# Kernel tuning notes

Measured on AMD Instinct MI355X. Metric: run time of the kernel, lower is better.

The kernel has to match this reference:

```python
import jax, jax.numpy as jnp
import numpy as np

N = 50000      # num nodes
E = 800000     # num edges
IN_C = 256
OUT_C = 128


def setup_inputs() -> dict:
    key = jax.random.key(0)
    k1, k2, k3, k4 = jax.random.split(key, 4)
    x = jax.random.normal(k1, (N, IN_C), dtype=jnp.float32)
    edge_index = jax.random.randint(k2, (2, E), 0, N, dtype=jnp.int64)
    # Linear params (Kaiming-uniform-ish scale like torch Linear reset)
    bound = 1.0 / np.sqrt(IN_C)
    W = jax.random.uniform(k3, (OUT_C, IN_C), minval=-bound, maxval=bound, dtype=jnp.float32)
    b = jax.random.uniform(k4, (OUT_C,), minval=-bound, maxval=bound, dtype=jnp.float32)
    return {"x": x, "edge_index": edge_index, "W": W, "b": b}


def reference(x, edge_index, W, b):
    # out = Linear(x): [N, OUT_C]
    out = jnp.einsum("ni,oi->no", x, W) + b
    src, dst = edge_index[0], edge_index[1]
    # gather source features: [E, OUT_C]
    src_feat = out[src]
    # scatter-mean by destination node
    summed = jax.ops.segment_sum(src_feat, dst, num_segments=N)  # [N, OUT_C]
    counts = jax.ops.segment_sum(jnp.ones((E,), dtype=out.dtype), dst, num_segments=N)
    mean = summed / jnp.maximum(counts, 1.0)[:, None]
    return mean
```

## Files before the change

kernel.cpp:

```cpp
#include <hip/hip_runtime.h>

#define N_NODES 50000
#define N_EDGES 800000
#define IN_CH   256
#define OUT_C H_unused 0
#undef OUT_C
#define OUT_CH  128

#define NB        391
#define CAP       3072
#define L1_CHUNK  2048
#define GBM       64
#define NGEMM     ((N_NODES + GBM - 1) / GBM)

typedef __attribute__((ext_vector_type(8))) short short8;
typedef __attribute__((ext_vector_type(4))) float f32x4;

__device__ __forceinline__ short f2bf(float f) {
    unsigned u = __float_as_uint(f);
    unsigned r = (u + 0x7fffu + ((u >> 16) & 1u)) >> 16;
    return (short)r;
}

__global__ __launch_bounds__(256) void convert_w(const float* __restrict__ W,
                                                 short* __restrict__ Wbf,
                                                 int* __restrict__ bcnt) {
    int t = blockIdx.x * 256 + threadIdx.x;
    const float* wp = W + t * 8;
    float4 v0 = ((const float4*)wp)[0];
    float4 v1 = ((const float4*)wp)[1];
    short8 s;
    s[0]=f2bf(v0.x); s[1]=f2bf(v0.y); s[2]=f2bf(v0.z); s[3]=f2bf(v0.w);
    s[4]=f2bf(v1.x); s[5]=f2bf(v1.y); s[6]=f2bf(v1.z); s[7]=f2bf(v1.w);
    *(short8*)&Wbf[t * 8] = s;
    if (t < NB) bcnt[t] = 0;
}

#define GBK 32
#define LDK 40
__global__ __launch_bounds__(256) void gemm_bucket(const float* __restrict__ x,
                                                   const short* __restrict__ Wbf,
                                                   const float* __restrict__ bias,
                                                   short* __restrict__ linbf,
                                                   const int* __restrict__ src,
                                                   const int* __restrict__ dst,
                                                   int* __restrict__ bcnt,
                                                   unsigned* __restrict__ rec) {
    __shared__ __align__(16) char smem[15360];
    const int tid = threadIdx.x;

    if (blockIdx.x < NGEMM) {
        short* As = (short*)smem;
        short* Bs = (short*)(smem + 5120);

        const int m0  = blockIdx.x * GBM;
        const int w    = tid >> 6;
        const int lane = tid & 63;
        const int lm   = lane & 15;
        const int lq   = lane >> 4;
        const int wrow = (w >> 1) * 32;
        const int wcol = (w & 1) * 64;

        f32x4 acc[2][4];
#pragma unroll
        for (int i = 0; i < 2; ++i)
#pragma unroll
            for (int j = 0; j < 4; ++j) acc[i][j] = (f32x4)(0.0f);

        const int arow = tid >> 2;
        const int aq   = tid & 3;
        const int brow = tid >> 1;
        const int bhalf = tid & 1;

        for (int k0 = 0; k0 < IN_CH; k0 += GBK) {
            {
                float4 v0 = make_float4(0.f,0.f,0.f,0.f), v1 = v0;
                if (m0 + arow < N_NODES) {
                    const float* xp = x + (size_t)(m0 + arow) * IN_CH + k0 + aq * 8;
                    v0 = ((const float4*)xp)[0];
                    v1 = ((const float4*)xp)[1];
                }
                short8 s;
                s[0]=f2bf(v0.x); s[1]=f2bf(v0.y); s[2]=f2bf(v0.z); s[3]=f2bf(v0.w);
                s[4]=f2bf(v1.x); s[5]=f2bf(v1.y); s[6]=f2bf(v1.z); s[7]=f2bf(v1.w);
                *(short8*)&As[arow * LDK + aq * 8] = s;
            }
            {
                const short* wp = Wbf + (size_t)brow * IN_CH + k0 + bhalf * 16;
                *(short8*)&Bs[brow * LDK + bhalf * 16]     = ((const short8*)wp)[0];
                *(short8*)&Bs[brow * LDK + bhalf * 16 + 8] = ((const short8*)wp)[1];
            }
            __syncthreads();

            short8 af[2], bfr[4];
#pragma unroll
            for (int rt = 0; rt < 2; ++rt)
                af[rt] = *(const short8*)&As[(wrow + rt * 16 + lm) * LDK + lq * 8];
#pragma unroll
            for (int ct = 0; ct < 4; ++ct)
                bfr[ct] = *(const short8*)&Bs[(wcol + ct * 16 + lm) * LDK + lq * 8];
#pragma unroll
            for (int rt = 0; rt < 2; ++rt)
#pragma unroll
                for (int ct = 0; ct < 4; ++ct)
                    acc[rt][ct] = __builtin_amdgcn_mfma_f32_16x16x32_bf16(
                        af[rt], bfr[ct], acc[rt][ct], 0, 0, 0);
            __syncthreads();
        }

#pragma unroll
        for (int ct = 0; ct < 4; ++ct) {
            int gcol = wcol + ct * 16 + lm;
            float bv = bias[gcol];
#pragma unroll
            for (int rt = 0; rt < 2; ++rt) {
#pragma unroll
                for (int r = 0; r < 4; ++r) {
                    int grow = m0 + wrow + rt * 16 + lq * 4 + r;
                    if (grow < N_NODES)
                        linbf[(size_t)grow * OUT_CH + gcol] = f2bf(acc[rt][ct][r] + bv);
                }
            }
        }
    } else {
        int* lhist       = (int*)smem;
        int* lscan       = (int*)(smem + 1568);
        int* lbase       = (int*)(smem + 3136);
        unsigned* staged = (unsigned*)(smem + 4704);

        const int blk = blockIdx.x - NGEMM;
        const int e0  = blk * L1_CHUNK;
        const int total = min(L1_CHUNK, N_EDGES - e0);

        for (int i = tid; i < NB; i += 256) lhist[i] = 0;
        __syncthreads();

        unsigned mypk[8];
        int myr[8];
        int myb[8];
#pragma unroll
        for (int j = 0; j < 8; ++j) {
            int i = tid + j * 256;
            myb[j] = -1;
            if (i < total) {
                unsigned d = (unsigned)dst[e0 + i];
                unsigned s = (unsigned)src[e0 + i];
                int b = (int)(d >> 7);
                myb[j] = b;
                mypk[j] = s | ((d & 127u) << 16) | ((unsigned)b << 23);
                myr[j] = atomicAdd(&lhist[b], 1);
            }
        }
        __syncthreads();

        if (tid < 64) {
            int carry = 0;
            for (int c = 0; c < NB; c += 64) {
                int idx = c + tid;
                int v = (idx < NB) ? lhist[idx] : 0;
                int incl = v;
#pragma unroll
                for (int s = 1; s < 64; s <<= 1) {
                    int t = __shfl_up(incl, s, 64);
                    if (tid >= s) incl += t;
                }
                if (idx < NB) lscan[idx] = carry + incl - v;
                carry += __shfl(incl, 63, 64);
            }
        }
        __syncthreads();

        for (int bkt = tid; bkt < NB; bkt += 256) {
            int c = lhist[bkt];
            lbase[bkt] = c ? atomicAdd(&bcnt[bkt], c) : 0;
        }
#pragma unroll
        for (int j = 0; j < 8; ++j) {
            if (myb[j] >= 0)
                staged[lscan[myb[j]] + myr[j]] = mypk[j];
        }
        __syncthreads();

        for (int p = tid; p < total; p += 256) {
            unsigned r = staged[p];
            int b = (int)(r >> 23);
            int gpos = lbase[b] + (p - lscan[b]);
            if (gpos < CAP)
                rec[(size_t)b * CAP + gpos] = r;
        }
    }
}

#define FG_THR 256
#define QCAP   1024
__global__ __launch_bounds__(FG_THR) void fine_gather(const int* __restrict__ bcnt,
                                                      const unsigned* __restrict__ rec,
                                                      const short* __restrict__ linbf,
                                                      float* __restrict__ out) {
    __shared__ unsigned short ssrc[QCAP];
    __shared__ int fh[32], fo[32], fc[32];

    const int tid = threadIdx.x;
    const int b   = blockIdx.x >> 2;
    const int q   = blockIdx.x & 3;
    const int lo  = q * 32;
    const int cnt = min(bcnt[b], CAP);
    const unsigned* rp = rec + (size_t)b * CAP;

    if (tid < 32) fh[tid] = 0;
    __syncthreads();

    for (int i = tid; i < cnt; i += FG_THR) {
        int f = (int)((rp[i] >> 16) & 127u) - lo;
        if ((unsigned)f < 32u) atomicAdd(&fh[f], 1);
    }
    __syncthreads();

    if (tid < 32) {
        int v = fh[tid], incl = v;
#pragma unroll
        for (int s = 1; s < 32; s <<= 1) {
            int t = __shfl_up(incl, s, 32);
            if (tid >= s) incl += t;
        }
        fo[tid] = incl - v;
        fc[tid] = incl - v;
    }
    __syncthreads();

    for (int i = tid; i < cnt; i += FG_THR) {
        unsigned r = rp[i];
        int f = (int)((r >> 16) & 127u) - lo;
        if ((unsigned)f < 32u) {
            int p = atomicAdd(&fc[f], 1);
            if (p < QCAP) ssrc[p] = (unsigned short)(r & 0xffffu);
        }
    }
    __syncthreads();

    const int l = tid & 15;
#pragma unroll 1
    for (int g = 0; g < 2; ++g) {
        int fn = g * 16 + (tid >> 4);
        int n = b * 128 + lo + fn;
        if (n >= N_NODES) continue;
        const int beg = fo[fn];
        const int deg = fh[fn];
        const int end = beg + deg;

        float a[8];
#pragma unroll
        for (int j = 0; j < 8; ++j) a[j] = 0.0f;

        int i = beg;
        for (; i + 3 < end; i += 4) {
            uint4 u[4];
#pragma unroll
            for (int e = 0; e < 4; ++e) {
                int s = ssrc[i + e];
                u[e] = *(const uint4*)&linbf[(size_t)s * OUT_CH + l * 8];
            }
#pragma unroll
            for (int e = 0; e < 4; ++e) {
                const unsigned* p = (const unsigned*)&u[e];
#pragma unroll
                for (int j = 0; j < 4; ++j) {
                    a[2*j]   += __uint_as_float(p[j] << 16);
                    a[2*j+1] += __uint_as_float(p[j] & 0xffff0000u);
                }
            }
        }
        for (; i < end; ++i) {
            int s = ssrc[i];
            uint4 u0 = *(const uint4*)&linbf[(size_t)s * OUT_CH + l * 8];
            const unsigned* p0 = (const unsigned*)&u0;
#pragma unroll
            for (int j = 0; j < 4; ++j) {
                a[2*j]   += __uint_as_float(p0[j] << 16);
                a[2*j+1] += __uint_as_float(p0[j] & 0xffff0000u);
            }
        }
        float inv = 1.0f / (float)(deg > 1 ? deg : 1);
        float4 o0, o1;
        o0.x = a[0]*inv; o0.y = a[1]*inv; o0.z = a[2]*inv; o0.w = a[3]*inv;
        o1.x = a[4]*inv; o1.y = a[5]*inv; o1.z = a[6]*inv; o1.w = a[7]*inv;
        float* op = &out[(size_t)n * OUT_CH + l * 8];
        ((float4*)op)[0] = o0;
        ((float4*)op)[1] = o1;
    }
}

extern "C" void kernel_launch(void* const* d_in, const int* in_sizes, int n_in,
                              void* d_out, int out_size, void* d_ws, size_t ws_size,
                              hipStream_t stream) {
    const float* x  = (const float*)d_in[0];
    const int*   ei = (const int*)d_in[1];
    const float* W  = (const float*)d_in[2];
    const float* b  = (const float*)d_in[3];
    float* out = (float*)d_out;

    const int* src = ei;
    const int* dst = ei + N_EDGES;

    char* ws = (char*)d_ws;
    short*    linbf = (short*)ws;    ws += ((size_t)N_NODES * OUT_CH * sizeof(short) + 255) & ~255ull;
    short*    Wbf   = (short*)ws;    ws += ((size_t)IN_CH * OUT_CH * sizeof(short) + 255) & ~255ull;
    unsigned* rec   = (unsigned*)ws; ws += ((size_t)NB * CAP * sizeof(unsigned) + 255) & ~255ull;
    int*      bcnt  = (int*)ws;

    convert_w<<<16, 256, 0, stream>>>(W, Wbf, bcnt);
    gemm_bucket<<<NGEMM + NB, 256, 0, stream>>>(x, Wbf, b, linbf, src, dst, bcnt, rec);
    fine_gather<<<NB * 4, FG_THR, 0, stream>>>(bcnt, rec, linbf, out);
}
```

Measured before the change: 145.4 us.

## Fuse GEMM, bucketing and gather into one cooperative persistent kernel

Replaces the three launches (weight conversion, GEMM plus edge bucketing, fine gather) with one persistent cooperative kernel of 512 blocks. The blocks loop over the GEMM tiles and bucket chunks, synchronise the whole grid, then loop over the gather work. Weights are now converted to bf16 inline in every GEMM tile instead of once up front, and the bucket counters are zeroed with a memset. This removes launch gaps but adds a grid-wide barrier, repeated W conversion, and fewer concurrent blocks than the original grids had.

Measured after the change: 345.1 us. +137.4%, slower.

```diff
diff --git a/kernel.cpp b/kernel.cpp
--- a/kernel.cpp
+++ b/kernel.cpp
@@ -1,17 +1,24 @@
 #include <hip/hip_runtime.h>
+#include <hip/hip_cooperative_groups.h>
+
+namespace cg = cooperative_groups;
 
 #define N_NODES 50000
 #define N_EDGES 800000
 #define IN_CH   256
-#define OUT_C H_unused 0
-#undef OUT_C
 #define OUT_CH  128
 
 #define NB        391
 #define CAP       3072
 #define L1_CHUNK  2048
+#define NBUK      ((N_EDGES + L1_CHUNK - 1) / L1_CHUNK)
 #define GBM       64
 #define NGEMM     ((N_NODES + GBM - 1) / GBM)
+#define GBK 32
+#define LDK 40
+
+#define GRID   512
+#define QCAP   1024
 
 typedef __attribute__((ext_vector_type(8))) short short8;
 typedef __attribute__((ext_vector_type(4))) float f32x4;
@@ -22,271 +29,270 @@
     return (short)r;
 }
 
-__global__ __launch_bounds__(256) void convert_w(const float* __restrict__ W,
-                                                 short* __restrict__ Wbf,
-                                                 int* __restrict__ bcnt) {
-    int t = blockIdx.x * 256 + threadIdx.x;
-    const float* wp = W + t * 8;
-    float4 v0 = ((const float4*)wp)[0];
-    float4 v1 = ((const float4*)wp)[1];
-    short8 s;
-    s[0]=f2bf(v0.x); s[1]=f2bf(v0.y); s[2]=f2bf(v0.z); s[3]=f2bf(v0.w);
-    s[4]=f2bf(v1.x); s[5]=f2bf(v1.y); s[6]=f2bf(v1.z); s[7]=f2bf(v1.w);
-    *(short8*)&Wbf[t * 8] = s;
-    if (t < NB) bcnt[t] = 0;
-}
-
-#define GBK 32
-#define LDK 40
-__global__ __launch_bounds__(256) void gemm_bucket(const float* __restrict__ x,
-                                                   const short* __restrict__ Wbf,
-                                                   const float* __restrict__ bias,
-                                                   short* __restrict__ linbf,
-                                                   const int* __restrict__ src,
-                                                   const int* __restrict__ dst,
-                                                   int* __restrict__ bcnt,
-                                                   unsigned* __restrict__ rec) {
+__global__ __launch_bounds__(256, 2) void fused(const float* __restrict__ x,
+                                                const float* __restrict__ W,
+                                                const float* __restrict__ bias,
+                                                short* __restrict__ linbf,
+                                                const int* __restrict__ src,
+                                                const int* __restrict__ dst,
+                                                int* __restrict__ bcnt,
+                                                unsigned* __restrict__ rec,
+                                                float* __restrict__ out) {
     __shared__ __align__(16) char smem[15360];
     const int tid = threadIdx.x;
 
-    if (blockIdx.x < NGEMM) {
-        short* As = (short*)smem;
-        short* Bs = (short*)(smem + 5120);
-
-        const int m0  = blockIdx.x * GBM;
-        const int w    = tid >> 6;
-        const int lane = tid & 63;
-        const int lm   = lane & 15;
-        const int lq   = lane >> 4;
-        const int wrow = (w >> 1) * 32;
-        const int wcol = (w & 1) * 64;
-
-        f32x4 acc[2][4];
-#pragma unroll
-        for (int i = 0; i < 2; ++i)
-#pragma unroll
-            for (int j = 0; j < 4; ++j) acc[i][j] = (f32x4)(0.0f);
-
-        const int arow = tid >> 2;
-        const int aq   = tid & 3;
-        const int brow = tid >> 1;
-        const int bhalf = tid & 1;
-
-        for (int k0 = 0; k0 < IN_CH; k0 += GBK) {
-            {
-                float4 v0 = make_float4(0.f,0.f,0.f,0.f), v1 = v0;
-                if (m0 + arow < N_NODES) {
-                    const float* xp = x + (size_t)(m0 + arow) * IN_CH + k0 + aq * 8;
-                    v0 = ((const float4*)xp)[0];
-                    v1 = ((const float4*)xp)[1];
-                }
-                short8 s;
-                s[0]=f2bf(v0.x); s[1]=f2bf(v0.y); s[2]=f2bf(v0.z); s[3]=f2bf(v0.w);
-                s[4]=f2bf(v1.x); s[5]=f2bf(v1.y); s[6]=f2bf(v1.z); s[7]=f2bf(v1.w);
-                *(short8*)&As[arow * LDK + aq * 8] = s;
-            }
-            {
-                const short* wp = Wbf + (size_t)brow * IN_CH + k0 + bhalf * 16;
-                *(short8*)&Bs[brow * LDK + bhalf * 16]     = ((const short8*)wp)[0];
-                *(short8*)&Bs[brow * LDK + bhalf * 16 + 8] = ((const short8*)wp)[1];
-            }
-            __syncthreads();
-
-            short8 af[2], bfr[4];
-#pragma unroll
-            for (int rt = 0; rt < 2; ++rt)
-                af[rt] = *(const short8*)&As[(wrow + rt * 16 + lm) * LDK + lq * 8];
-#pragma unroll
-            for (int ct = 0; ct < 4; ++ct)
-                bfr[ct] = *(const short8*)&Bs[(wcol + ct * 16 + lm) * LDK + lq * 8];
-#pragma unroll
-            for (int rt = 0; rt < 2; ++rt)
+    for (int item = blockIdx.x; item < NGEMM + NBUK; item += GRID) {
+        if (item < NGEMM) {
+            short* As = (short*)smem;
+            short* Bs = (short*)(smem + 5120);
+
+            const int m0  = item * GBM;
+            const int w    = tid >> 6;
+            const int lane = tid & 63;
+            const int lm   = lane & 15;
+            const int lq   = lane >> 4;
+            const int wrow = (w >> 1) * 32;
+            const int wcol = (w & 1) * 64;
+
+            f32x4 acc[2][4];
+#pragma unroll
+            for (int i = 0; i < 2; ++i)
+#pragma unroll
+                for (int j = 0; j < 4; ++j) acc[i][j] = (f32x4)(0.0f);
+
+            const int arow = tid >> 2;
+            const int aq   = tid & 3;
+            const int brow = tid >> 1;
+            const int bhalf = tid & 1;
+
+            for (int k0 = 0; k0 < IN_CH; k0 += GBK) {
+                {
+                    float4 v0 = make_float4(0.f,0.f,0.f,0.f), v1 = v0;
+                    if (m0 + arow < N_NODES) {
+                        const float* xp = x + (size_t)(m0 + arow) * IN_CH + k0 + aq * 8;
+                        v0 = ((const float4*)xp)[0];
+                        v1 = ((const float4*)xp)[1];
+                    }
+                    short8 s;
+                    s[0]=f2bf(v0.x); s[1]=f2bf(v0.y); s[2]=f2bf(v0.z); s[3]=f2bf(v0.w);
+                    s[4]=f2bf(v1.x); s[5]=f2bf(v1.y); s[6]=f2bf(v1.z); s[7]=f2bf(v1.w);
+                    *(short8*)&As[arow * LDK + aq * 8] = s;
+                }
+                {
+                    const float* wp = W + (size_t)brow * IN_CH + k0 + bhalf * 16;
+                    float4 w0 = ((const float4*)wp)[0];
+                    float4 w1 = ((const float4*)wp)[1];
+                    float4 w2 = ((const float4*)wp)[2];
+                    float4 w3 = ((const float4*)wp)[3];
+                    short8 s0, s1;
+                    s0[0]=f2bf(w0.x); s0[1]=f2bf(w0.y); s0[2]=f2bf(w0.z); s0[3]=f2bf(w0.w);
+                    s0[4]=f2bf(w1.x); s0[5]=f2bf(w1.y); s0[6]=f2bf(w1.z); s0[7]=f2bf(w1.w);
+                    s1[0]=f2bf(w2.x); s1[1]=f2bf(w2.y); s1[2]=f2bf(w2.z); s1[3]=f2bf(w2.w);
+                    s1[4]=f2bf(w3.x); s1[5]=f2bf(w3.y); s1[6]=f2bf(w3.z); s1[7]=f2bf(w3.w);
+                    *(short8*)&Bs[brow * LDK + bhalf * 16]     = s0;
+                    *(short8*)&Bs[brow * LDK + bhalf * 16 + 8] = s1;
+                }
+                __syncthreads();
+
+                short8 af[2], bfr[4];
+#pragma unroll
+                for (int rt = 0; rt < 2; ++rt)
+                    af[rt] = *(const short8*)&As[(wrow + rt * 16 + lm) * LDK + lq * 8];
 #pragma unroll
                 for (int ct = 0; ct < 4; ++ct)
-                    acc[rt][ct] = __builtin_amdgcn_mfma_f32_16x16x32_bf16(
-                        af[rt], bfr[ct], acc[rt][ct], 0, 0, 0);
-            __syncthreads();
-        }
-
-#pragma unroll
-        for (int ct = 0; ct < 4; ++ct) {
-            int gcol = wcol + ct * 16 + lm;
-            float bv = bias[gcol];
-#pragma unroll
-            for (int rt = 0; rt < 2; ++rt) {
-#pragma unroll
-                for (int r = 0; r < 4; ++r) {
-                    int grow = m0 + wrow + rt * 16 + lq * 4 + r;
-                    if (grow < N_NODES)
-                        linbf[(size_t)grow * OUT_CH + gcol] = f2bf(acc[rt][ct][r] + bv);
-                }
-            }
-        }
-    } else {
-        int* lhist       = (int*)smem;
-        int* lscan       = (int*)(smem + 1568);
-        int* lbase       = (int*)(smem + 3136);
-        unsigned* staged = (unsigned*)(smem + 4704);
-
-        const int blk = blockIdx.x - NGEMM;
-        const int e0  = blk * L1_CHUNK;
-        const int total = min(L1_CHUNK, N_EDGES - e0);
-
-        for (int i = tid; i < NB; i += 256) lhist[i] = 0;
-        __syncthreads();
-
-        unsigned mypk[8];
-        int myr[8];
-        int myb[8];
-#pragma unroll
-        for (int j = 0; j < 8; ++j) {
-            int i = tid + j * 256;
-            myb[j] = -1;
-            if (i < total) {
-                unsigned d = (unsigned)dst[e0 + i];
-                unsigned s = (unsigned)src[e0 + i];
-                int b = (int)(d >> 7);
-                myb[j] = b;
-                mypk[j] = s | ((d & 127u) << 16) | ((unsigned)b << 23);
-                myr[j] = atomicAdd(&lhist[b], 1);
+                    bfr[ct] = *(const short8*)&Bs[(wcol + ct * 16 + lm) * LDK + lq * 8];
+#pragma unroll
+                for (int rt = 0; rt < 2; ++rt)
+#pragma unroll
+                    for (int ct = 0; ct < 4; ++ct)
+                        acc[rt][ct] = __builtin_amdgcn_mfma_f32_16x16x32_bf16(
+                            af[rt], bfr[ct], acc[rt][ct], 0, 0, 0);
+                __syncthreads();
+            }
+
+#pragma unroll
+            for (int ct = 0; ct < 4; ++ct) {
+                int gcol = wcol + ct * 16 + lm;
+                float bv = bias[gcol];
+#pragma unroll
+                for (int rt = 0; rt < 2; ++rt) {
+#pragma unroll
+                    for (int r = 0; r < 4; ++r) {
+                        int grow = m0 + wrow + rt * 16 + lq * 4 + r;
+                        if (grow < N_NODES)
+                            linbf[(size_t)grow * OUT_CH + gcol] = f2bf(acc[rt][ct][r] + bv);
+                    }
+                }
+            }
+        } else {
+            int* lhist       = (int*)smem;
+            int* lscan       = (int*)(smem + 1568);
+            int* lbase       = (int*)(smem + 3136);
+            unsigned* staged = (unsigned*)(smem + 4704);
+
+            const int blk = item - NGEMM;
+            const int e0  = blk * L1_CHUNK;
+            const int total = min(L1_CHUNK, N_EDGES - e0);
+
+            for (int i = tid; i < NB; i += 256) lhist[i] = 0;
+            __syncthreads();
+
+            unsigned mypk[8];
+            int myr[8];
+            int myb[8];
+#pragma unroll
+            for (int j = 0; j < 8; ++j) {
+                int i = tid + j * 256;
+                myb[j] = -1;
+                if (i < total) {
+                    unsigned d = (unsigned)dst[e0 + i];
+                    unsigned s = (unsigned)src[e0 + i];
+                    int b = (int)(d >> 7);
+                    myb[j] = b;
+                    mypk[j] = s | ((d & 127u) << 16) | ((unsigned)b << 23);
+                    myr[j] = atomicAdd(&lhist[b], 1);
+                }
+            }
+            __syncthreads();
+
+            if (tid < 64) {
+                int carry = 0;
+                for (int c = 0; c < NB; c += 64) {
+                    int idx = c + tid;
+                    int v = (idx < NB) ? lhist[idx] : 0;
+                    int incl = v;
+#pragma unroll
+                    for (int s = 1; s < 64; s <<= 1) {
+                        int t = __shfl_up(incl, s, 64);
+                        if (tid >= s) incl += t;
+                    }
+                    if (idx < NB) lscan[idx] = carry + incl - v;
+                    carry += __shfl(incl, 63, 64);
+                }
+            }
+            __syncthreads();
+
+            for (int bkt = tid; bkt < NB; bkt += 256) {
+                int c = lhist[bkt];
+                lbase[bkt] = c ? atomicAdd(&bcnt[bkt], c) : 0;
+            }
+#pragma unroll
+            for (int j = 0; j < 8; ++j) {
+                if (myb[j] >= 0)
+                    staged[lscan[myb[j]] + myr[j]] = mypk[j];
+            }
+            __syncthreads();
+
+            for (int p = tid; p < total; p += 256) {
+                unsigned r = staged[p];
+                int b = (int)(r >> 23);
+                int gpos = lbase[b] + (p - lscan[b]);
+                if (gpos < CAP)
+                    rec[(size_t)b * CAP + gpos] = r;
             }
         }
         __syncthreads();
-
-        if (tid < 64) {
-            int carry = 0;
-            for (int c = 0; c < NB; c += 64) {
-                int idx = c + tid;
-                int v = (idx < NB) ? lhist[idx] : 0;
-                int incl = v;
-#pragma unroll
-                for (int s = 1; s < 64; s <<= 1) {
-                    int t = __shfl_up(incl, s, 64);
+    }
+
+    __threadfence();
+    cg::this_grid().sync();
+    __threadfence();
+
+    {
+        unsigned short* ssrc = (unsigned short*)smem;
+        int* fh = (int*)(smem + 2048);
+        int* fo = (int*)(smem + 2176);
+        int* fc = (int*)(smem + 2304);
+
+        for (int qq = blockIdx.x; qq < NB * 4; qq += GRID) {
+            const int b  = qq >> 2;
+            const int lo = (qq & 3) * 32;
+            const int cnt = min(bcnt[b], CAP);
+            const unsigned* rp = rec + (size_t)b * CAP;
+
+            __syncthreads();
+            if (tid < 32) fh[tid] = 0;
+            __syncthreads();
+
+            for (int i = tid; i < cnt; i += 256) {
+                int f = (int)((rp[i] >> 16) & 127u) - lo;
+                if ((unsigned)f < 32u) atomicAdd(&fh[f], 1);
+            }
+            __syncthreads();
+
+            if (tid < 32) {
+                int v = fh[tid], incl = v;
+#pragma unroll
+                for (int s = 1; s < 32; s <<= 1) {
+                    int t = __shfl_up(incl, s, 32);
                     if (tid >= s) incl += t;
                 }
-                if (idx < NB) lscan[idx] = carry + incl - v;
-                carry += __shfl(incl, 63, 64);
+                fo[tid] = incl - v;
+                fc[tid] = incl - v;
+            }
+            __syncthreads();
+
+            for (int i = tid; i < cnt; i += 256) {
+                unsigned r = rp[i];
+                int f = (int)((r >> 16) & 127u) - lo;
+                if ((unsigned)f < 32u) {
+                    int p = atomicAdd(&fc[f], 1);
+                    if (p < QCAP) ssrc[p] = (unsigned short)(r & 0xffffu);
+                }
+            }
+            __syncthreads();
+
+            const int l = tid & 15;
+#pragma unroll 1
+            for (int g = 0; g < 2; ++g) {
+                int fn = g * 16 + (tid >> 4);
+                int n = b * 128 + lo + fn;
+                if (n >= N_NODES) continue;
+                const int beg = fo[fn];
+                const int deg = fh[fn];
+                const int end = beg + deg;
+
+                float a[8];
+#pragma unroll
+                for (int j = 0; j < 8; ++j) a[j] = 0.0f;
+
+                int i = beg;
+                for (; i + 3 < end; i += 4) {
+                    uint4 u[4];
+#pragma unroll
+                    for (int e = 0; e < 4; ++e) {
+                        int s = ssrc[i + e];
+                        u[e] = *(const uint4*)&linbf[(size_t)s * OUT_CH + l * 8];
+                    }
+#pragma unroll
+                    for (int e = 0; e < 4; ++e) {
+                        const unsigned* p = (const unsigned*)&u[e];
+#pragma unroll
+                        for (int j = 0; j < 4; ++j) {
+                            a[2*j]   += __uint_as_float(p[j] << 16);
+                            a[2*j+1] += __uint_as_float(p[j] & 0xffff0000u);
+                        }
+                    }
+                }
+                for (; i < end; ++i) {
+                    int s = ssrc[i];
+                    uint4 u0 = *(const uint4*)&linbf[(size_t)s * OUT_CH + l * 8];
+                    const unsigned* p0 = (const unsigned*)&u0;
+#pragma unroll
+                    for (int j = 0; j < 4; ++j) {
+                        a[2*j]   += __uint_as_float(p0[j] << 16);
+                        a[2*j+1] += __uint_as_float(p0[j] & 0xffff0000u);
+                    }
+                }
+                float inv = 1.0f / (float)(deg > 1 ? deg : 1);
+                float4 o0, o1;
+                o0.x = a[0]*inv; o0.y = a[1]*inv; o0.z = a[2]*inv; o0.w = a[3]*inv;
+                o1.x = a[4]*inv; o1.y = a[5]*inv; o1.z = a[6]*inv; o1.w = a[7]*inv;
+                float* op = &out[(size_t)n * OUT_CH + l * 8];
+                ((float4*)op)[0] = o0;
+                ((float4*)op)[1] = o1;
             }
         }
-        __syncthreads();
-
-        for (int bkt = tid; bkt < NB; bkt += 256) {
-            int c = lhist[bkt];
-            lbase[bkt] = c ? atomicAdd(&bcnt[bkt], c) : 0;
-        }
-#pragma unroll
-        for (int j = 0; j < 8; ++j) {
-            if (myb[j] >= 0)
-                staged[lscan[myb[j]] + myr[j]] = mypk[j];
-        }
-        __syncthreads();
-
-        for (int p = tid; p < total; p += 256) {
-            unsigned r = staged[p];
-            int b = (int)(r >> 23);
-            int gpos = lbase[b] + (p - lscan[b]);
-            if (gpos < CAP)
-                rec[(size_t)b * CAP + gpos] = r;
-        }
-    }
-}
-
-#define FG_THR 256
-#define QCAP   1024
-__global__ __launch_bounds__(FG_THR) void fine_gather(const int* __restrict__ bcnt,
-                                                      const unsigned* __restrict__ rec,
-                                                      const short* __restrict__ linbf,
-                                                      float* __restrict__ out) {
-    __shared__ unsigned short ssrc[QCAP];
-    __shared__ int fh[32], fo[32], fc[32];
-
-    const int tid = threadIdx.x;
-    const int b   = blockIdx.x >> 2;
-    const int q   = blockIdx.x & 3;
-    const int lo  = q * 32;
-    const int cnt = min(bcnt[b], CAP);
-    const unsigned* rp = rec + (size_t)b * CAP;
-
-    if (tid < 32) fh[tid] = 0;
-    __syncthreads();
-
-    for (int i = tid; i < cnt; i += FG_THR) {
-        int f = (int)((rp[i] >> 16) & 127u) - lo;
-        if ((unsigned)f < 32u) atomicAdd(&fh[f], 1);
-    }
-    __syncthreads();
-
-    if (tid < 32) {
-        int v = fh[tid], incl = v;
-#pragma unroll
-        for (int s = 1; s < 32; s <<= 1) {
-            int t = __shfl_up(incl, s, 32);
-            if (tid >= s) incl += t;
-        }
-        fo[tid] = incl - v;
-        fc[tid] = incl - v;
-    }
-    __syncthreads();
-
-    for (int i = tid; i < cnt; i += FG_THR) {
-        unsigned r = rp[i];
-        int f = (int)((r >> 16) & 127u) - lo;
-        if ((unsigned)f < 32u) {
-            int p = atomicAdd(&fc[f], 1);
-            if (p < QCAP) ssrc[p] = (unsigned short)(r & 0xffffu);
-        }
-    }
-    __syncthreads();
-
-    const int l = tid & 15;
-#pragma unroll 1
-    for (int g = 0; g < 2; ++g) {
-        int fn = g * 16 + (tid >> 4);
-        int n = b * 128 + lo + fn;
-        if (n >= N_NODES) continue;
-        const int beg = fo[fn];
-        const int deg = fh[fn];
-        const int end = beg + deg;
-
-        float a[8];
-#pragma unroll
-        for (int j = 0; j < 8; ++j) a[j] = 0.0f;
-
-        int i = beg;
-        for (; i + 3 < end; i += 4) {
-            uint4 u[4];
-#pragma unroll
-            for (int e = 0; e < 4; ++e) {
-                int s = ssrc[i + e];
-                u[e] = *(const uint4*)&linbf[(size_t)s * OUT_CH + l * 8];
-            }
-#pragma unroll
-            for (int e = 0; e < 4; ++e) {
-                const unsigned* p = (const unsigned*)&u[e];
-#pragma unroll
-                for (int j = 0; j < 4; ++j) {
-                    a[2*j]   += __uint_as_float(p[j] << 16);
-                    a[2*j+1] += __uint_as_float(p[j] & 0xffff0000u);
-                }
-            }
-        }
-        for (; i < end; ++i) {
-            int s = ssrc[i];
-            uint4 u0 = *(const uint4*)&linbf[(size_t)s * OUT_CH + l * 8];
-            const unsigned* p0 = (const unsigned*)&u0;
-#pragma unroll
-            for (int j = 0; j < 4; ++j) {
-                a[2*j]   += __uint_as_float(p0[j] << 16);
-                a[2*j+1] += __uint_as_float(p0[j] & 0xffff0000u);
-            }
-        }
-        float inv = 1.0f / (float)(deg > 1 ? deg : 1);
-        float4 o0, o1;
-        o0.x = a[0]*inv; o0.y = a[1]*inv; o0.z = a[2]*inv; o0.w = a[3]*inv;
-        o1.x = a[4]*inv; o1.y = a[5]*inv; o1.z = a[6]*inv; o1.w = a[7]*inv;
-        float* op = &out[(size_t)n * OUT_CH + l * 8];
-        ((float4*)op)[0] = o0;
-        ((float4*)op)[1] = o1;
     }
 }
 
@@ -296,7 +302,7 @@
     const float* x  = (const float*)d_in[0];
     const int*   ei = (const int*)d_in[1];
     const float* W  = (const float*)d_in[2];
-    const float* b  = (const float*)d_in[3];
+    const float* bs = (const float*)d_in[3];
     float* out = (float*)d_out;
 
     const int* src = ei;
@@ -304,11 +310,14 @@
 
     char* ws = (char*)d_ws;
     short*    linbf = (short*)ws;    ws += ((size_t)N_NODES * OUT_CH * sizeof(short) + 255) & ~255ull;
-    short*    Wbf   = (short*)ws;    ws += ((size_t)IN_CH * OUT_CH * sizeof(short) + 255) & ~255ull;
     unsigned* rec   = (unsigned*)ws; ws += ((size_t)NB * CAP * sizeof(unsigned) + 255) & ~255ull;
     int*      bcnt  = (int*)ws;
 
-    convert_w<<<16, 256, 0, stream>>>(W, Wbf, bcnt);
-    gemm_bucket<<<NGEMM + NB, 256, 0, stream>>>(x, Wbf, b, linbf, src, dst, bcnt, rec);
-    fine_gather<<<NB * 4, FG_THR, 0, stream>>>(bcnt, rec, linbf, out);
+    hipMemsetAsync(bcnt, 0, 512 * sizeof(int), stream);
+
+    void* kargs[] = {(void*)&x, (void*)&W, (void*)&bs, (void*)&linbf,
+                     (void*)&src, (void*)&dst, (void*)&bcnt, (void*)&rec,
+                     (void*)&out};
+    hipLaunchCooperativeKernel((void*)fused, dim3(GRID), dim3(256),
+                               kargs, 0, stream);
 }
```
